# Kernel tuning notes

Hardware: AMD Instinct MI355X
Metric: run time of the kernel (lower is better)

Reference implementation:

```python
import jax, jax.numpy as jnp
import numpy as np

N = 100_000      # nodes
E = 1_600_000    # directed edges (before self-loops)
F_IN = 256       # input node features
H = 128          # hidden_dim
HEADS = 2
C_HEAD = H // HEADS  # 64, GATConv out_channels per head
G = 128          # graphs in batch
NCLS = 10
NEG_SLOPE = 0.2  # PyG GATConv default


def setup_inputs() -> dict:
    key = jax.random.key(0)
    ks = jax.random.split(key, 20)
    p = lambda k, shape: (jax.random.normal(k, shape, jnp.float32) * 0.05)
    x = jax.random.normal(ks[0], (N, F_IN), jnp.float32)
    edge_index = jax.random.randint(ks[1], (2, E), 0, N, dtype=jnp.int64)
    batch = jnp.sort(jax.random.randint(ks[2], (N,), 0, G, dtype=jnp.int64))
    return dict(
        x=x, edge_index=edge_index, batch=batch,
        pre_w=p(ks[3], (F_IN, H)), pre_b=p(ks[4], (H,)),
        w1=p(ks[5], (H, H)), asrc1=p(ks[6], (HEADS, C_HEAD)), adst1=p(ks[7], (HEADS, C_HEAD)), b1=p(ks[8], (H,)),
        w2=p(ks[9], (H, H)), asrc2=p(ks[10], (HEADS, C_HEAD)), adst2=p(ks[11], (HEADS, C_HEAD)), b2=p(ks[12], (H,)),
        post_w1=p(ks[13], (H, H)), post_b1=p(ks[14], (H,)),
        post_w2=p(ks[15], (H, NCLS)), post_b2=p(ks[16], (NCLS,)),
    )


def _gat_conv(h_in, w, a_src, a_dst, b, src, dst):
    # h: [N, heads, c]
    h = (h_in @ w).reshape(N, HEADS, C_HEAD)
    alpha_src = jnp.sum(h * a_src, axis=-1)  # [N, heads]
    alpha_dst = jnp.sum(h * a_dst, axis=-1)  # [N, heads]
    e = jax.nn.leaky_relu(alpha_src[src] + alpha_dst[dst], NEG_SLOPE)  # [E+N, heads]
    # numerically stable softmax over incoming edges of each destination node
    m = jax.ops.segment_max(e, dst, num_segments=N)
    ex = jnp.exp(e - m[dst])
    denom = jax.ops.segment_sum(ex, dst, num_segments=N)
    alpha = ex / denom[dst]                                           # [E+N, heads]
    out = jax.ops.segment_sum(h[src] * alpha[:, :, None], dst, num_segments=N)
    return out.reshape(N, H) + b  # concat heads + bias


def reference(x, edge_index, batch, pre_w, pre_b,
              w1, asrc1, adst1, b1, w2, asrc2, adst2, b2,
              post_w1, post_b1, post_w2, post_b2):
    # PyG GATConv default add_self_loops=True
    loop = jnp.arange(N, dtype=edge_index.dtype)
    src = jnp.concatenate([edge_index[0], loop])
    dst = jnp.concatenate([edge_index[1], loop])

    h = jax.nn.relu(x @ pre_w + pre_b)
    reprs = jax.ops.segment_sum(h, batch, num_segments=G)
    h = jax.nn.relu(_gat_conv(h, w1, asrc1, adst1, b1, src, dst))
    reprs = reprs + jax.ops.segment_sum(h, batch, num_segments=G)
    h = jax.nn.relu(_gat_conv(h, w2, asrc2, adst2, b2, src, dst))
    reprs = reprs + jax.ops.segment_sum(h, batch, num_segments=G)
    z = jax.nn.relu(reprs @ post_w1 + post_b1) @ post_w2 + post_b2
    return jax.nn.log_softmax(z, axis=-1)
```

## Files before the change

kernel.cpp:

```cpp
#include <hip/hip_runtime.h>
#include <hip/hip_bf16.h>
#include <math.h>

#define NNODES 100000
#define NEDGES 1600000
#define FIN 256
#define HDIM 128
#define NGRAPH 128
#define NCLS 10
#define NEG 0.2f

#define NBUCK 98
#define EPB 4096
#define EBLK ((NEDGES + EPB - 1) / EPB)

typedef short bf8 __attribute__((ext_vector_type(8)));
typedef float f4 __attribute__((ext_vector_type(4)));

__device__ __forceinline__ float lrelu(float x) { return x > 0.f ? x : NEG * x; }

__device__ __forceinline__ unsigned short f2bf(float f) {
  union { float f; unsigned int u; } v; v.f = f;
  unsigned int r = v.u + 0x7fffu + ((v.u >> 16) & 1u);
  return (unsigned short)(r >> 16);
}
__device__ __forceinline__ float bf2f(unsigned short u) {
  union { unsigned int u; float f; } v; v.u = ((unsigned int)u) << 16; return v.f;
}
__device__ __forceinline__ float bf_lo(unsigned int p) {
  union { unsigned int u; float f; } v; v.u = p << 16; return v.f;
}
__device__ __forceinline__ float bf_hi(unsigned int p) {
  union { unsigned int u; float f; } v; v.u = p & 0xffff0000u; return v.f;
}

__global__ __launch_bounds__(256) void convert_transpose(const float* __restrict__ w,
                                                         unsigned short* __restrict__ wt,
                                                         int K) {
  int i = blockIdx.x * 256 + threadIdx.x;
  if (i >= K * 128) return;
  int k = i >> 7, n = i & 127;
  wt[n * K + k] = f2bf(w[(size_t)k * 128 + n]);
}

__global__ __launch_bounds__(256) void gemm_mfma(const void* __restrict__ Av,
                                                 int a_bf16,
                                                 const unsigned short* __restrict__ Bt,
                                                 const float* __restrict__ bias,
                                                 unsigned short* __restrict__ Cb,
                                                 unsigned int* __restrict__ Cp,
                                                 const float* __restrict__ a_src,
                                                 const float* __restrict__ a_dst,
                                                 float* __restrict__ o_as,
                                                 float* __restrict__ o_ad,
                                                 int M, int K, int dorelu) {
  __shared__ bf8 As[512];
  __shared__ bf8 Bs[512];
  int tid = threadIdx.x;
  int wv = tid >> 6, lane = tid & 63;
  int quad = lane >> 4, m16 = lane & 15;
  int row0 = blockIdx.x * 128;

  int l0 = tid & 63, t0 = tid >> 6, t1 = t0 + 4;
  int rA0 = row0 + t0 * 16 + (l0 & 15); if (rA0 > M - 1) rA0 = M - 1;
  int rA1 = row0 + t1 * 16 + (l0 & 15); if (rA1 > M - 1) rA1 = M - 1;
  int nB0 = t0 * 16 + (l0 & 15);
  int nB1 = t1 * 16 + (l0 & 15);
  int cOff = (l0 >> 4) * 8;

  float4 fA0a, fA0b, fA1a, fA1b;
  bf8 hA0, hA1, pB0, pB1;

  auto loadA = [&](int kb) {
    if (a_bf16) {
      const unsigned short* base = (const unsigned short*)Av;
      hA0 = *reinterpret_cast<const bf8*>(base + (size_t)rA0 * K + kb + cOff);
      hA1 = *reinterpret_cast<const bf8*>(base + (size_t)rA1 * K + kb + cOff);
    } else {
      const float* base = (const float*)Av;
      const float* p0 = base + (size_t)rA0 * K + kb + cOff;
      const float* p1 = base + (size_t)rA1 * K + kb + cOff;
      fA0a = *reinterpret_cast<const float4*>(p0);
      fA0b = *reinterpret_cast<const float4*>(p0 + 4);
      fA1a = *reinterpret_cast<const float4*>(p1);
      fA1b = *reinterpret_cast<const float4*>(p1 + 4);
    }
  };
  auto loadB = [&](int kb) {
    pB0 = *reinterpret_cast<const bf8*>(&Bt[(size_t)nB0 * K + kb + cOff]);
    pB1 = *reinterpret_cast<const bf8*>(&Bt[(size_t)nB1 * K + kb + cOff]);
  };
  auto cvt8 = [&](float4 a, float4 b) -> bf8 {
    bf8 v;
    v[0] = (short)f2bf(a.x); v[1] = (short)f2bf(a.y);
    v[2] = (short)f2bf(a.z); v[3] = (short)f2bf(a.w);
    v[4] = (short)f2bf(b.x); v[5] = (short)f2bf(b.y);
    v[6] = (short)f2bf(b.z); v[7] = (short)f2bf(b.w);
    return v;
  };

  f4 acc[2][8];
#pragma unroll
  for (int a = 0; a < 2; ++a)
#pragma unroll
    for (int b = 0; b < 8; ++b) acc[a][b] = (f4){0.f, 0.f, 0.f, 0.f};

  loadA(0); loadB(0);
  for (int kb = 0; kb < K; kb += 32) {
    __syncthreads();
    if (a_bf16) { As[tid] = hA0; As[tid + 256] = hA1; }
    else        { As[tid] = cvt8(fA0a, fA0b); As[tid + 256] = cvt8(fA1a, fA1b); }
    Bs[tid] = pB0; Bs[tid + 256] = pB1;
    __syncthreads();
    int kn = kb + 32;
    if (kn < K) { loadA(kn); loadB(kn); }
    bf8 af0 = As[(wv * 2 + 0) * 64 + lane];
    bf8 af1 = As[(wv * 2 + 1) * 64 + lane];
#pragma unroll
    for (int tn = 0; tn < 8; ++tn) {
      bf8 bfm = Bs[tn * 64 + lane];
      acc[0][tn] = __builtin_amdgcn_mfma_f32_16x16x32_bf16(af0, bfm, acc[0][tn], 0, 0, 0);
      acc[1][tn] = __builtin_amdgcn_mfma_f32_16x16x32_bf16(af1, bfm, acc[1][tn], 0, 0, 0);
    }
  }

  if (Cp) {
    if (a_src) {
      float aS[8], aD[8];
#pragma unroll
      for (int tn = 0; tn < 4; ++tn) {
        aS[tn]     = a_src[tn * 16 + m16];
        aS[tn + 4] = a_src[64 + tn * 16 + m16];
        aD[tn]     = a_dst[tn * 16 + m16];
        aD[tn + 4] = a_dst[64 + tn * 16 + m16];
      }
#pragma unroll
      for (int mt = 0; mt < 2; ++mt)
#pragma unroll
        for (int r = 0; r < 4; ++r) {
          int row = row0 + wv * 32 + mt * 16 + quad * 4 + r;
          float ps0 = 0.f, ps1 = 0.f, pd0 = 0.f, pd1 = 0.f;
#pragma unroll
          for (int tn = 0; tn < 4; ++tn) {
            float v0 = acc[mt][tn][r], v1 = acc[mt][tn + 4][r];
            ps0 = fmaf(v0, aS[tn], ps0);
            ps1 = fmaf(v1, aS[tn + 4], ps1);
            pd0 = fmaf(v0, aD[tn], pd0);
            pd1 = fmaf(v1, aD[tn + 4], pd1);
          }
#pragma unroll
          for (int o = 8; o; o >>= 1) {
            ps0 += __shfl_xor(ps0, o); ps1 += __shfl_xor(ps1, o);
            pd0 += __shfl_xor(pd0, o); pd1 += __shfl_xor(pd1, o);
          }
          if (m16 == 0 && row < M) {
            o_as[2 * row] = ps0; o_as[2 * row + 1] = ps1;
            o_ad[2 * row] = pd0; o_ad[2 * row + 1] = pd1;
          }
        }
    }
#pragma unroll
    for (int mt = 0; mt < 2; ++mt)
#pragma unroll
      for (int tn = 0; tn < 4; ++tn)
#pragma unroll
        for (int r = 0; r < 4; ++r) {
          int row = row0 + wv * 32 + mt * 16 + quad * 4 + r;
          if (row < M) {
            unsigned int p = (unsigned int)f2bf(acc[mt][tn][r]) |
                             ((unsigned int)f2bf(acc[mt][tn + 4][r]) << 16);
            Cp[(size_t)row * 64 + tn * 16 + m16] = p;
          }
        }
  } else {
#pragma unroll
    for (int mt = 0; mt < 2; ++mt)
#pragma unroll
      for (int tn = 0; tn < 8; ++tn) {
        float bv = bias ? bias[tn * 16 + m16] : 0.f;
#pragma unroll
        for (int r = 0; r < 4; ++r) {
          int row = row0 + wv * 32 + mt * 16 + quad * 4 + r;
          if (row < M) {
            float v = acc[mt][tn][r] + bv;
            if (dorelu) v = fmaxf(v, 0.f);
            Cb[(size_t)row * 128 + tn * 16 + m16] = f2bf(v);
          }
        }
      }
  }
}

__global__ void find_starts(const int* __restrict__ batch, int* __restrict__ gstart) {
  int g = threadIdx.x;
  if (g > NGRAPH) return;
  if (g == NGRAPH) { gstart[g] = NNODES; return; }
  int lo = 0, hi = NNODES;
  while (lo < hi) { int mid = (lo + hi) >> 1; if (batch[mid] < g) lo = mid + 1; else hi = mid; }
  gstart[g] = lo;
}

__global__ __launch_bounds__(256) void bin_count(const int* __restrict__ edst,
                                                 int* __restrict__ blockHist) {
  __shared__ int hist[NBUCK];
  int t = threadIdx.x, blk = blockIdx.x;
  if (t < NBUCK) hist[t] = 0;
  __syncthreads();
  int e0 = blk * EPB;
#pragma unroll
  for (int it = 0; it < EPB / 256; ++it) {
    int e = e0 + it * 256 + t;
    if (e < NEDGES) atomicAdd(&hist[((unsigned)edst[e]) >> 10], 1);
  }
  __syncthreads();
  if (t < NBUCK) blockHist[blk * NBUCK + t] = hist[t];
}

__global__ __launch_bounds__(512) void colscan(const int* __restrict__ blockHist,
                                               int* __restrict__ blockBaseCol,
                                               int* __restrict__ bucket_total) {
  __shared__ int s[512];
  int b = blockIdx.x, t = threadIdx.x;
  int v = (t < EBLK) ? blockHist[t * NBUCK + b] : 0;
  s[t] = v;
  __syncthreads();
  for (int off = 1; off < 512; off <<= 1) {
    int u = (t >= off) ? s[t - off] : 0;
    __syncthreads();
    s[t] += u;
    __syncthreads();
  }
  if (t < EBLK) blockBaseCol[b * EBLK + t] = s[t] - v;
  if (t == 511) bucket_total[b] = s[511];
}

__global__ __launch_bounds__(128) void bscan(const int* __restrict__ bucket_total,
                                             int* __restrict__ bucket_ptr) {
  __shared__ int s[128];
  int t = threadIdx.x;
  int v = (t < NBUCK) ? bucket_total[t] : 0;
  s[t] = v;
  __syncthreads();
  for (int off = 1; off < 128; off <<= 1) {
    int u = (t >= off) ? s[t - off] : 0;
    __syncthreads();
    s[t] += u;
    __syncthreads();
  }
  if (t < NBUCK) bucket_ptr[t] = s[t] - v;
  if (t == 127) bucket_ptr[NBUCK] = s[127];
}

__global__ __launch_bounds__(512) void bin_place(const int* __restrict__ esrc,
                                                 const int* __restrict__ edst,
                                                 const int* __restrict__ blockBaseCol,
                                                 const int* __restrict__ bucket_ptr,
                                                 unsigned* __restrict__ stagingG) {
  __shared__ int hist[NBUCK + 1], lbase[NBUCK + 1], lcur[NBUCK + 1], cbase[NBUCK];
  __shared__ int tmp[128];
  __shared__ uint2 st[EPB];
  int t = threadIdx.x, blk = blockIdx.x;
  if (t < NBUCK + 1) hist[t] = 0;
  __syncthreads();
  int e0 = blk * EPB;
#pragma unroll
  for (int it = 0; it < EPB / 512; ++it) {
    int e = e0 + it * 512 + t;
    int b = NBUCK;
    if (e < NEDGES) b = ((unsigned)edst[e]) >> 10;
    atomicAdd(&hist[b], 1);
  }
  __syncthreads();
  if (t < 128) tmp[t] = (t < NBUCK + 1) ? hist[t] : 0;
  __syncthreads();
  for (int off = 1; off < 128; off <<= 1) {
    int u = 0;
    if (t < 128 && t >= off) u = tmp[t - off];
    __syncthreads();
    if (t < 128) tmp[t] += u;
    __syncthreads();
  }
  if (t < NBUCK + 1) { int ex = tmp[t] - hist[t]; lbase[t] = ex; lcur[t] = ex; }
  if (t < NBUCK) cbase[t] = bucket_ptr[t] + blockBaseCol[t * EBLK + blk];
  __syncthreads();
#pragma unroll
  for (int it = 0; it < EPB / 512; ++it) {
    int e = e0 + it * 512 + t;
    unsigned s = 0, d = 0xFFFFFFFFu;
    if (e < NEDGES) { s = (unsigned)esrc[e]; d = (unsigned)edst[e]; }
    int b = (d == 0xFFFFFFFFu) ? NBUCK : (int)(d >> 10);
    int slot = atomicAdd(&lcur[b], 1);
    st[slot] = make_uint2(s, d);
  }
  __syncthreads();
  for (int i = t; i < EPB; i += 512) {
    uint2 ed = st[i];
    if (ed.y == 0xFFFFFFFFu) continue;
    int b = (int)(ed.y >> 10);
    stagingG[cbase[b] + (i - lbase[b])] = ((ed.y & 1023u) << 17) | ed.x;
  }
}

__global__ __launch_bounds__(1024) void bucket_csr_fused(const unsigned* __restrict__ stagingG,
                                                         const int* __restrict__ bucket_ptr,
                                                         int* __restrict__ row_ptr,
                                                         int* __restrict__ colv) {
  __shared__ int dl[1024];
  __shared__ int cur[1024];
  int b = blockIdx.x, t = threadIdx.x;
  dl[t] = 0;
  __syncthreads();
  int s0 = bucket_ptr[b], s1 = bucket_ptr[b + 1];
  for (int j = s0 + t; j < s1; j += 1024)
    atomicAdd(&dl[stagingG[j] >> 17], 1);
  __syncthreads();
  int myDeg = dl[t];
  for (int off = 1; off < 1024; off <<= 1) {
    int u = (t >= off) ? dl[t - off] : 0;
    __syncthreads();
    dl[t] += u;
    __syncthreads();
  }
  int rp = s0 + dl[t] - myDeg;
  cur[t] = rp;
  int n = (b << 10) + t;
  if (n < NNODES) row_ptr[n] = rp;
  if (n == NNODES - 1) row_ptr[NNODES] = rp + myDeg;
  __syncthreads();
  for (int j = s0 + t; j < s1; j += 1024) {
    unsigned v = stagingG[j];
    int pos = atomicAdd(&cur[v >> 17], 1);
    colv[pos] = (int)(v & 0x1FFFFu);
  }
}

template<int T>
__device__ __forceinline__ void gather_T(const unsigned int* __restrict__ hwb,
                                         int lane, int sl, float w0l, float w1l,
                                         float& acc0, float& acc1) {
#pragma unroll
  for (int t = 0; t < T; ++t) {
    int s = __builtin_amdgcn_readlane(sl, t);
    float w0 = __uint_as_float(__builtin_amdgcn_readlane(__float_as_uint(w0l), t));
    float w1 = __uint_as_float(__builtin_amdgcn_readlane(__float_as_uint(w1l), t));
    unsigned q = hwb[(size_t)s * 64 + lane];
    acc0 = fmaf(w0, bf_lo(q), acc0);
    acc1 = fmaf(w1, bf_hi(q), acc1);
  }
}

__global__ __launch_bounds__(256) void aggregate(const unsigned int* __restrict__ hwb,
                                                 const float* __restrict__ a_s,
                                                 const float* __restrict__ a_d,
                                                 const int* __restrict__ row_ptr,
                                                 const int* __restrict__ colv,
                                                 const float* __restrict__ bias,
                                                 unsigned short* __restrict__ out) {
  int i = (blockIdx.x * 256 + threadIdx.x) >> 6;
  int lane = threadIdx.x & 63;
  if (i >= NNODES) return;
  float ad0 = a_d[2 * i], ad1 = a_d[2 * i + 1];
  float es0 = lrelu(a_s[2 * i] + ad0), es1 = lrelu(a_s[2 * i + 1] + ad1);
  int start = row_ptr[i], end = row_ptr[i + 1];
  int deg = end - start;

  int sl = 0; float e0l = -1e30f, e1l = -1e30f;
  if (lane < deg) {
    sl = colv[start + lane];
    float2 av = *reinterpret_cast<const float2*>(&a_s[2 * sl]);
    e0l = lrelu(av.x + ad0); e1l = lrelu(av.y + ad1);
  }
  float m0 = fmaxf(es0, e0l), m1 = fmaxf(es1, e1l);
  for (int j = start + 64 + lane; j < end; j += 64) {
    int s = colv[j];
    float2 av = *reinterpret_cast<const float2*>(&a_s[2 * s]);
    m0 = fmaxf(m0, lrelu(av.x + ad0));
    m1 = fmaxf(m1, lrelu(av.y + ad1));
  }
  for (int o = 32; o; o >>= 1) {
    m0 = fmaxf(m0, __shfl_xor(m0, o));
    m1 = fmaxf(m1, __shfl_xor(m1, o));
  }
  float w0l = lane < deg ? __expf(e0l - m0) : 0.f;
  float w1l = lane < deg ? __expf(e1l - m1) : 0.f;
  float d0 = w0l, d1 = w1l;
  for (int o = 32; o; o >>= 1) { d0 += __shfl_xor(d0, o); d1 += __shfl_xor(d1, o); }
  float ws0 = __expf(es0 - m0), ws1 = __expf(es1 - m1);
  float den0 = d0 + ws0, den1 = d1 + ws1;

  unsigned int ps = hwb[(size_t)i * 64 + lane];
  float acc0 = ws0 * bf_lo(ps), acc1 = ws1 * bf_hi(ps);
  int dmin = deg < 64 ? deg : 64;
  switch ((dmin + 7) >> 3) {
    case 1: gather_T<8 >(hwb, lane, sl, w0l, w1l, acc0, acc1); break;
    case 2: gather_T<16>(hwb, lane, sl, w0l, w1l, acc0, acc1); break;
    case 3: gather_T<24>(hwb, lane, sl, w0l, w1l, acc0, acc1); break;
    case 4: gather_T<32>(hwb, lane, sl, w0l, w1l, acc0, acc1); break;
    case 5: gather_T<40>(hwb, lane, sl, w0l, w1l, acc0, acc1); break;
    case 6: gather_T<48>(hwb, lane, sl, w0l, w1l, acc0, acc1); break;
    case 7: gather_T<56>(hwb, lane, sl, w0l, w1l, acc0, acc1); break;
    case 8: gather_T<64>(hwb, lane, sl, w0l, w1l, acc0, acc1); break;
    default: break;
  }
  for (int j = start + 64; j < end; ++j) {
    int s = colv[j];
    float2 av = *reinterpret_cast<const float2*>(&a_s[2 * s]);
    float w0 = __expf(lrelu(av.x + ad0) - m0);
    float w1 = __expf(lrelu(av.y + ad1) - m1);
    den0 += w0; den1 += w1;
    unsigned int q = hwb[(size_t)s * 64 + lane];
    acc0 = fmaf(w0, bf_lo(q), acc0);
    acc1 = fmaf(w1, bf_hi(q), acc1);
  }
  out[(size_t)i * 128 + lane]      = f2bf(fmaxf(acc0 / den0 + bias[lane], 0.f));
  out[(size_t)i * 128 + 64 + lane] = f2bf(fmaxf(acc1 / den1 + bias[64 + lane], 0.f));
}

#define SEG_CHUNK 128
__global__ __launch_bounds__(128) void seg_sum_fast(const unsigned short* __restrict__ h,
                                                    const int* __restrict__ batch,
                                                    const int* __restrict__ gstart,
                                                    float* __restrict__ reprs) {
  int n0 = blockIdx.x * SEG_CHUNK;
  if (n0 >= NNODES) return;
  int nend = n0 + SEG_CHUNK; if (nend > NNODES) nend = NNODES;
  int tid = threadIdx.x;
  int r = n0;
  while (r < nend) {
    int g = batch[r];
    int segend = gstart[g + 1]; if (segend > nend) segend = nend;
    float a0 = 0.f, a1 = 0.f, a2 = 0.f, a3 = 0.f;
    for (; r + 3 < segend; r += 4) {
      a0 += bf2f(h[(size_t)r * 128 + tid]);
      a1 += bf2f(h[(size_t)(r + 1) * 128 + tid]);
      a2 += bf2f(h[(size_t)(r + 2) * 128 + tid]);
      a3 += bf2f(h[(size_t)(r + 3) * 128 + tid]);
    }
    for (; r < segend; ++r) a0 += bf2f(h[(size_t)r * 128 + tid]);
    atomicAdd(&reprs[g * 128 + tid], (a0 + a1) + (a2 + a3));
  }
}

__global__ __launch_bounds__(128) void head_kernel(const float* __restrict__ reprs,
                                                   const float* __restrict__ pw1,
                                                   const float* __restrict__ pb1,
                                                   const float* __restrict__ pw2,
                                                   const float* __restrict__ pb2,
                                                   float* __restrict__ out) {
  __shared__ float r[128], t1[128], z[NCLS];
  int g = blockIdx.x, tid = threadIdx.x;
  r[tid] = reprs[g * 128 + tid];
  __syncthreads();
  float acc = pb1[tid];
  for (int k = 0; k < 128; ++k) acc = fmaf(r[k], pw1[k * 128 + tid], acc);
  t1[tid] = fmaxf(acc, 0.f);
  __syncthreads();
  if (tid < NCLS) {
    float zz = pb2[tid];
    for (int k = 0; k < 128; ++k) zz = fmaf(t1[k], pw2[k * NCLS + tid], zz);
    z[tid] = zz;
  }
  __syncthreads();
  if (tid == 0) {
    float mx = -1e30f;
    for (int c = 0; c < NCLS; ++c) mx = fmaxf(mx, z[c]);
    float s = 0.f;
    for (int c = 0; c < NCLS; ++c) s += expf(z[c] - mx);
    float ls = logf(s) + mx;
    for (int c = 0; c < NCLS; ++c) out[g * NCLS + c] = z[c] - ls;
  }
}

extern "C" void kernel_launch(void* const* d_in, const int* in_sizes, int n_in,
                              void* d_out, int out_size, void* d_ws, size_t ws_size,
                              hipStream_t stream) {
  const float* x     = (const float*)d_in[0];
  const int*   eidx  = (const int*)d_in[1];
  const int*   batch = (const int*)d_in[2];
  const float* pre_w = (const float*)d_in[3];
  const float* pre_b = (const float*)d_in[4];
  const float* w1    = (const float*)d_in[5];
  const float* asrc1 = (const float*)d_in[6];
  const float* adst1 = (const float*)d_in[7];
  const float* b1    = (const float*)d_in[8];
  const float* w2    = (const float*)d_in[9];
  const float* asrc2 = (const float*)d_in[10];
  const float* adst2 = (const float*)d_in[11];
  const float* b2    = (const float*)d_in[12];
  const float* pw1   = (const float*)d_in[13];
  const float* pb1   = (const float*)d_in[14];
  const float* pw2   = (const float*)d_in[15];
  const float* pb2   = (const float*)d_in[16];
  float* out = (float*)d_out;

  const int* esrc = eidx;
  const int* edst = eidx + NEDGES;

  char* wsp = (char*)d_ws;
  size_t off = 0;
  auto alloc = [&](size_t bytes) -> void* {
    void* p = wsp + off;
    off += (bytes + 255) & ~(size_t)255;
    return p;
  };
  unsigned short* hb = (unsigned short*)alloc((size_t)NNODES * 128 * 2);
  unsigned int* hwb  = (unsigned int*)alloc((size_t)NNODES * 64 * 4);
  float* a_s         = (float*)alloc((size_t)NNODES * 2 * 4);
  float* a_d         = (float*)alloc((size_t)NNODES * 2 * 4);
  float* reprs       = (float*)alloc((size_t)NGRAPH * 128 * 4);
  int* gstart        = (int*)alloc((NGRAPH + 1) * 4);
  int* row_ptr       = (int*)alloc(((size_t)NNODES + 1) * 4);
  int* colv          = (int*)alloc((size_t)NEDGES * 4);
  unsigned short* wt_pre = (unsigned short*)alloc((size_t)128 * FIN * 2);
  unsigned short* wt1    = (unsigned short*)alloc((size_t)128 * HDIM * 2);
  unsigned short* wt2    = (unsigned short*)alloc((size_t)128 * HDIM * 2);
  int* blockHist     = (int*)alloc((size_t)EBLK * NBUCK * 4);
  int* blockBaseCol  = (int*)alloc((size_t)NBUCK * EBLK * 4);
  int* bucket_total  = (int*)alloc(NBUCK * 4);
  int* bucket_ptr    = (int*)alloc((NBUCK + 1) * 4);
  unsigned* stagingG = (unsigned*)alloc((size_t)NEDGES * 4);

  int wb = NNODES / 4;
  int sb = (NNODES + SEG_CHUNK - 1) / SEG_CHUNK;
  int gb = (NNODES + 127) / 128;

  convert_transpose<<<(FIN * 128 + 255) / 256, 256, 0, stream>>>(pre_w, wt_pre, FIN);
  convert_transpose<<<(HDIM * 128 + 255) / 256, 256, 0, stream>>>(w1, wt1, HDIM);
  convert_transpose<<<(HDIM * 128 + 255) / 256, 256, 0, stream>>>(w2, wt2, HDIM);

  hipMemsetAsync(reprs, 0, (size_t)NGRAPH * 128 * 4, stream);
  find_starts<<<1, 256, 0, stream>>>(batch, gstart);

  bin_count<<<EBLK, 256, 0, stream>>>(edst, blockHist);
  colscan<<<NBUCK, 512, 0, stream>>>(blockHist, blockBaseCol, bucket_total);
  bscan<<<1, 128, 0, stream>>>(bucket_total, bucket_ptr);
  bin_place<<<EBLK, 512, 0, stream>>>(esrc, edst, blockBaseCol, bucket_ptr, stagingG);
  bucket_csr_fused<<<NBUCK, 1024, 0, stream>>>(stagingG, bucket_ptr, row_ptr, colv);

  gemm_mfma<<<gb, 256, 0, stream>>>(x, 0, wt_pre, pre_b, hb, nullptr,
                                    nullptr, nullptr, nullptr, nullptr, NNODES, FIN, 1);
  seg_sum_fast<<<sb, 128, 0, stream>>>(hb, batch, gstart, reprs);

  gemm_mfma<<<gb, 256, 0, stream>>>(hb, 1, wt1, nullptr, nullptr, hwb,
                                    asrc1, adst1, a_s, a_d, NNODES, HDIM, 0);
  aggregate<<<wb, 256, 0, stream>>>(hwb, a_s, a_d, row_ptr, colv, b1, hb);
  seg_sum_fast<<<sb, 128, 0, stream>>>(hb, batch, gstart, reprs);

  gemm_mfma<<<gb, 256, 0, stream>>>(hb, 1, wt2, nullptr, nullptr, hwb,
                                    asrc2, adst2, a_s, a_d, NNODES, HDIM, 0);
  aggregate<<<wb, 256, 0, stream>>>(hwb, a_s, a_d, row_ptr, colv, b2, hb);
  seg_sum_fast<<<sb, 128, 0, stream>>>(hb, batch, gstart, reprs);

  head_kernel<<<NGRAPH, 128, 0, stream>>>(reprs, pw1, pb1, pw2, pb2, out);
}
```

Baseline: 505.7 us.

## Halve GEMM block tile to 64 rows and double-buffer global prefetch

The MFMA GEMM now gives each block 64 rows instead of 128, so each wave owns one 16-row strip. The grid doubles to about 1563 blocks, which should fill the CUs better. Global loads are now prefetched two k-steps ahead into register double buffers, to hide load latency behind the MFMAs. In exchange, B-tile reuse per block drops and the B weights are reloaded twice as often across the grid, while register pressure shifts from accumulators to prefetch buffers.

```diff
diff --git a/kernel.cpp b/kernel.cpp
--- a/kernel.cpp
+++ b/kernel.cpp
@@ -54,41 +54,31 @@
                                                  float* __restrict__ o_as,
                                                  float* __restrict__ o_ad,
                                                  int M, int K, int dorelu) {
-  __shared__ bf8 As[512];
+  __shared__ bf8 As[256];
   __shared__ bf8 Bs[512];
   int tid = threadIdx.x;
   int wv = tid >> 6, lane = tid & 63;
   int quad = lane >> 4, m16 = lane & 15;
-  int row0 = blockIdx.x * 128;
-
-  int l0 = tid & 63, t0 = tid >> 6, t1 = t0 + 4;
-  int rA0 = row0 + t0 * 16 + (l0 & 15); if (rA0 > M - 1) rA0 = M - 1;
-  int rA1 = row0 + t1 * 16 + (l0 & 15); if (rA1 > M - 1) rA1 = M - 1;
-  int nB0 = t0 * 16 + (l0 & 15);
-  int nB1 = t1 * 16 + (l0 & 15);
+  int row0 = blockIdx.x * 64;
+
+  int l0 = tid & 63;
+  int rA = row0 + (tid >> 6) * 16 + (l0 & 15); if (rA > M - 1) rA = M - 1;
+  int nB0 = (tid >> 6) * 16 + (l0 & 15);
+  int nB1 = (4 + (tid >> 6)) * 16 + (l0 & 15);
   int cOff = (l0 >> 4) * 8;
 
-  float4 fA0a, fA0b, fA1a, fA1b;
-  bf8 hA0, hA1, pB0, pB1;
-
-  auto loadA = [&](int kb) {
+  float4 fA[2][2]; bf8 hA[2]; bf8 pB[2][2];
+  auto loadTile = [&](int buf, int kb) {
     if (a_bf16) {
-      const unsigned short* base = (const unsigned short*)Av;
-      hA0 = *reinterpret_cast<const bf8*>(base + (size_t)rA0 * K + kb + cOff);
-      hA1 = *reinterpret_cast<const bf8*>(base + (size_t)rA1 * K + kb + cOff);
+      hA[buf] = *reinterpret_cast<const bf8*>(
+          (const unsigned short*)Av + (size_t)rA * K + kb + cOff);
     } else {
-      const float* base = (const float*)Av;
-      const float* p0 = base + (size_t)rA0 * K + kb + cOff;
-      const float* p1 = base + (size_t)rA1 * K + kb + cOff;
-      fA0a = *reinterpret_cast<const float4*>(p0);
-      fA0b = *reinterpret_cast<const float4*>(p0 + 4);
-      fA1a = *reinterpret_cast<const float4*>(p1);
-      fA1b = *reinterpret_cast<const float4*>(p1 + 4);
+      const float* p = (const float*)Av + (size_t)rA * K + kb + cOff;
+      fA[buf][0] = *reinterpret_cast<const float4*>(p);
+      fA[buf][1] = *reinterpret_cast<const float4*>(p + 4);
     }
-  };
-  auto loadB = [&](int kb) {
-    pB0 = *reinterpret_cast<const bf8*>(&Bt[(size_t)nB0 * K + kb + cOff]);
-    pB1 = *reinterpret_cast<const bf8*>(&Bt[(size_t)nB1 * K + kb + cOff]);
+    pB[buf][0] = *reinterpret_cast<const bf8*>(&Bt[(size_t)nB0 * K + kb + cOff]);
+    pB[buf][1] = *reinterpret_cast<const bf8*>(&Bt[(size_t)nB1 * K + kb + cOff]);
   };
   auto cvt8 = [&](float4 a, float4 b) -> bf8 {
     bf8 v;
@@ -99,29 +89,27 @@
     return v;
   };
 
-  f4 acc[2][8];
-#pragma unroll
-  for (int a = 0; a < 2; ++a)
-#pragma unroll
-    for (int b = 0; b < 8; ++b) acc[a][b] = (f4){0.f, 0.f, 0.f, 0.f};
-
-  loadA(0); loadB(0);
+  f4 acc[8];
+#pragma unroll
+  for (int b = 0; b < 8; ++b) acc[b] = (f4){0.f, 0.f, 0.f, 0.f};
+
+  loadTile(0, 0);
+  if (K > 32) loadTile(1, 32);
+  int cur = 0;
   for (int kb = 0; kb < K; kb += 32) {
     __syncthreads();
-    if (a_bf16) { As[tid] = hA0; As[tid + 256] = hA1; }
-    else        { As[tid] = cvt8(fA0a, fA0b); As[tid + 256] = cvt8(fA1a, fA1b); }
-    Bs[tid] = pB0; Bs[tid + 256] = pB1;
-    __syncthreads();
-    int kn = kb + 32;
-    if (kn < K) { loadA(kn); loadB(kn); }
-    bf8 af0 = As[(wv * 2 + 0) * 64 + lane];
-    bf8 af1 = As[(wv * 2 + 1) * 64 + lane];
+    As[tid] = a_bf16 ? hA[cur] : cvt8(fA[cur][0], fA[cur][1]);
+    Bs[tid] = pB[cur][0]; Bs[tid + 256] = pB[cur][1];
+    __syncthreads();
+    int kn = kb + 64;
+    if (kn < K) loadTile(cur, kn);
+    bf8 af = As[wv * 64 + lane];
 #pragma unroll
     for (int tn = 0; tn < 8; ++tn) {
       bf8 bfm = Bs[tn * 64 + lane];
-      acc[0][tn] = __builtin_amdgcn_mfma_f32_16x16x32_bf16(af0, bfm, acc[0][tn], 0, 0, 0);
-      acc[1][tn] = __builtin_amdgcn_mfma_f32_16x16x32_bf16(af1, bfm, acc[1][tn], 0, 0, 0);
+      acc[tn] = __builtin_amdgcn_mfma_f32_16x16x32_bf16(af, bfm, acc[tn], 0, 0, 0);
     }
+    cur ^= 1;
   }
 
   if (Cp) {
@@ -135,59 +123,53 @@
         aD[tn + 4] = a_dst[64 + tn * 16 + m16];
       }
 #pragma unroll
-      for (int mt = 0; mt < 2; ++mt)
-#pragma unroll
-        for (int r = 0; r < 4; ++r) {
-          int row = row0 + wv * 32 + mt * 16 + quad * 4 + r;
-          float ps0 = 0.f, ps1 = 0.f, pd0 = 0.f, pd1 = 0.f;
-#pragma unroll
-          for (int tn = 0; tn < 4; ++tn) {
-            float v0 = acc[mt][tn][r], v1 = acc[mt][tn + 4][r];
-            ps0 = fmaf(v0, aS[tn], ps0);
-            ps1 = fmaf(v1, aS[tn + 4], ps1);
-            pd0 = fmaf(v0, aD[tn], pd0);
-            pd1 = fmaf(v1, aD[tn + 4], pd1);
-          }
-#pragma unroll
-          for (int o = 8; o; o >>= 1) {
-            ps0 += __shfl_xor(ps0, o); ps1 += __shfl_xor(ps1, o);
-            pd0 += __shfl_xor(pd0, o); pd1 += __shfl_xor(pd1, o);
-          }
-          if (m16 == 0 && row < M) {
-            o_as[2 * row] = ps0; o_as[2 * row + 1] = ps1;
-            o_ad[2 * row] = pd0; o_ad[2 * row + 1] = pd1;
-          }
+      for (int r = 0; r < 4; ++r) {
+        int row = row0 + wv * 16 + quad * 4 + r;
+        float ps0 = 0.f, ps1 = 0.f, pd0 = 0.f, pd1 = 0.f;
+#pragma unroll
+        for (int tn = 0; tn < 4; ++tn) {
+          float v0 = acc[tn][r], v1 = acc[tn + 4][r];
+          ps0 = fmaf(v0, aS[tn], ps0);
+          ps1 = fmaf(v1, aS[tn + 4], ps1);
+          pd0 = fmaf(v0, aD[tn], pd0);
+          pd1 = fmaf(v1, aD[tn + 4], pd1);
         }
-    }
-#pragma unroll
-    for (int mt = 0; mt < 2; ++mt)
-#pragma unroll
-      for (int tn = 0; tn < 4; ++tn)
-#pragma unroll
-        for (int r = 0; r < 4; ++r) {
-          int row = row0 + wv * 32 + mt * 16 + quad * 4 + r;
-          if (row < M) {
-            unsigned int p = (unsigned int)f2bf(acc[mt][tn][r]) |
-                             ((unsigned int)f2bf(acc[mt][tn + 4][r]) << 16);
-            Cp[(size_t)row * 64 + tn * 16 + m16] = p;
-          }
+#pragma unroll
+        for (int o = 8; o; o >>= 1) {
+          ps0 += __shfl_xor(ps0, o); ps1 += __shfl_xor(ps1, o);
+          pd0 += __shfl_xor(pd0, o); pd1 += __shfl_xor(pd1, o);
         }
-  } else {
-#pragma unroll
-    for (int mt = 0; mt < 2; ++mt)
-#pragma unroll
-      for (int tn = 0; tn < 8; ++tn) {
-        float bv = bias ? bias[tn * 16 + m16] : 0.f;
-#pragma unroll
-        for (int r = 0; r < 4; ++r) {
-          int row = row0 + wv * 32 + mt * 16 + quad * 4 + r;
-          if (row < M) {
-            float v = acc[mt][tn][r] + bv;
-            if (dorelu) v = fmaxf(v, 0.f);
-            Cb[(size_t)row * 128 + tn * 16 + m16] = f2bf(v);
-          }
+        if (m16 == 0 && row < M) {
+          o_as[2 * row] = ps0; o_as[2 * row + 1] = ps1;
+          o_ad[2 * row] = pd0; o_ad[2 * row + 1] = pd1;
         }
       }
+    }
+#pragma unroll
+    for (int tn = 0; tn < 4; ++tn)
+#pragma unroll
+      for (int r = 0; r < 4; ++r) {
+        int row = row0 + wv * 16 + quad * 4 + r;
+        if (row < M) {
+          unsigned int p = (unsigned int)f2bf(acc[tn][r]) |
+                           ((unsigned int)f2bf(acc[tn + 4][r]) << 16);
+          Cp[(size_t)row * 64 + tn * 16 + m16] = p;
+        }
+      }
+  } else {
+#pragma unroll
+    for (int tn = 0; tn < 8; ++tn) {
+      float bv = bias ? bias[tn * 16 + m16] : 0.f;
+#pragma unroll
+      for (int r = 0; r < 4; ++r) {
+        int row = row0 + wv * 16 + quad * 4 + r;
+        if (row < M) {
+          float v = acc[tn][r] + bv;
+          if (dorelu) v = fmaxf(v, 0.f);
+          Cb[(size_t)row * 128 + tn * 16 + m16] = f2bf(v);
+        }
+      }
+    }
   }
 }
 
@@ -522,7 +504,7 @@
 
   int wb = NNODES / 4;
   int sb = (NNODES + SEG_CHUNK - 1) / SEG_CHUNK;
-  int gb = (NNODES + 127) / 128;
+  int gb = (NNODES + 63) / 64;
 
   convert_transpose<<<(FIN * 128 + 255) / 256, 256, 0, stream>>>(pre_w, wt_pre, FIN);
   convert_transpose<<<(HDIM * 128 + 255) / 256, 256, 0, stream>>>(w1, wt1, HDIM);
```

New measurement: 1.147 ms. 127% more time.
